# Kernel tuning notes

Measured on AMD Instinct MI355X. Metric: run time of the kernel, lower is better.

The kernel has to match this reference:

```python
import jax, jax.numpy as jnp
import numpy as np
import math

B, LQ, LK = 8, 1024, 1024
D_MODEL, NHEAD = 512, 8
DH = D_MODEL // NHEAD
FACTOR = 5
U = FACTOR * int(np.ceil(np.log(LQ)))  # 35: Informer's sample_k == n_top here (L_Q == L_K)


def _ln(x, g, b, eps=1e-5):
    m = x.mean(-1, keepdims=True)
    v = ((x - m) ** 2).mean(-1, keepdims=True)
    return (x - m) / jnp.sqrt(v + eps) * g + b


def _heads(x):  # (B,L,D) -> (B,H,L,Dh)
    Bx, L, _ = x.shape
    return x.reshape(Bx, L, NHEAD, DH).transpose(0, 2, 1, 3)


def _merge(x):  # (B,H,L,Dh) -> (B,L,D)
    Bx, H, L, Dh = x.shape
    return x.transpose(0, 2, 1, 3).reshape(Bx, L, H * Dh)


def _prob_attn(q, k, v, index_sample):
    # Informer ProbAttention, mask_flag=False. q,k,v: (B,H,L,Dh)
    Bx, H, Lq, Dh = q.shape
    Lk = k.shape[2]
    k_samp = k[:, :, index_sample, :]                        # (B,H,Lq,U,Dh) gathered keys
    qk_samp = jnp.einsum('bhld,bhlud->bhlu', q, k_samp)      # sampled scores
    M = qk_samp.max(-1) - qk_samp.sum(-1) / Lk               # sparsity measurement (B,H,Lq)
    _, top = jax.lax.top_k(M, U)                             # (B,H,U) top-u query indices
    q_red = jnp.take_along_axis(q, top[..., None], axis=2)   # (B,H,U,Dh)
    scores = jnp.einsum('bhud,bhkd->bhuk', q_red, k) * (1.0 / math.sqrt(Dh))
    attn = jax.nn.softmax(scores, axis=-1)
    upd = jnp.einsum('bhuk,bhkd->bhud', attn, v)             # (B,H,U,Dh)
    # initial context = mean of V (non-causal branch), then scatter top-u rows
    ctx = jnp.broadcast_to(v.mean(2, keepdims=True), (Bx, H, Lq, Dh))
    bi = jnp.arange(Bx)[:, None, None]
    hi = jnp.arange(H)[None, :, None]
    ctx = ctx.at[bi, hi, top].set(upd)
    return ctx


def _full_attn(q, k, v):
    s = jnp.einsum('bhld,bhsd->bhls', q, k) * (1.0 / math.sqrt(q.shape[-1]))
    a = jax.nn.softmax(s, axis=-1)
    return jnp.einsum('bhls,bhsd->bhld', a, v)


def setup_inputs():
    key = jax.random.key(0)
    ks = jax.random.split(key, 40)
    d = {}
    d['tgt'] = jax.random.normal(ks[0], (B, LQ, D_MODEL), jnp.float32)
    d['memory'] = jax.random.normal(ks[1], (B, LK, D_MODEL), jnp.float32)
    d['index_sample'] = jax.random.randint(ks[2], (LQ, U), 0, LK)
    i = 3
    for pre in ('1', '2'):
        for n in ('q', 'k', 'v', 'o'):
            d['w%s%s' % (n, pre)] = jax.random.normal(ks[i], (D_MODEL, D_MODEL), jnp.float32) * 0.02
            d['b%s%s' % (n, pre)] = jnp.zeros((D_MODEL,), jnp.float32)
            i += 1
    d['conv1_w'] = jax.random.normal(ks[i], (D_MODEL, 4 * D_MODEL), jnp.float32) * 0.02; i += 1
    d['conv1_b'] = jnp.zeros((4 * D_MODEL,), jnp.float32)
    d['conv2_w'] = jax.random.normal(ks[i], (4 * D_MODEL, D_MODEL), jnp.float32) * 0.02; i += 1
    d['conv2_b'] = jnp.zeros((D_MODEL,), jnp.float32)
    for n in ('ln1', 'ln2', 'ln3'):
        d[n + '_g'] = jnp.ones((D_MODEL,), jnp.float32)
        d[n + '_b'] = jnp.zeros((D_MODEL,), jnp.float32)
    return d


def reference(tgt, memory, index_sample, wq1, bq1, wk1, bk1, wv1, bv1, wo1, bo1,
              wq2, bq2, wk2, bk2, wv2, bv2, wo2, bo2,
              conv1_w, conv1_b, conv2_w, conv2_b,
              ln1_g, ln1_b, ln2_g, ln2_b, ln3_g, ln3_b):
    # dropout layers are identity (eval mode)
    x = tgt
    q = _heads(x @ wq1 + bq1)
    k = _heads(x @ wk1 + bk1)
    v = _heads(x @ wv1 + bv1)
    xn = _merge(_prob_attn(q, k, v, index_sample)) @ wo1 + bo1   # ProbSparse self-attn
    x = _ln(x + xn, ln1_g, ln1_b)                                # norm_enc1, with residual
    q = _heads(x @ wq2 + bq2)
    k = _heads(memory @ wk2 + bk2)
    v = _heads(memory @ wv2 + bv2)
    x = _merge(_full_attn(q, k, v)) @ wo2 + bo2                  # full cross-attn (no residual, per source)
    y = x = _ln(x, ln2_g, ln2_b)                                 # norm_enc2
    y = jax.nn.relu(y @ conv1_w + conv1_b) @ conv2_w + conv2_b   # conv1x1 FFN
    return _ln(x + y, ln3_g, ln3_b)                              # norm_enc3
```

## Files before the change

### kernel.cpp

```cpp
#include <hip/hip_runtime.h>
#include <hip/hip_bf16.h>
#include <cstdint>

constexpr int Bb  = 8;
constexpr int Ls  = 1024;
constexpr int DM  = 512;
constexpr int NH  = 8;
constexpr int DHd = 64;
constexpr int MR  = Bb * Ls;
constexpr int ZH  = Bb * NH;

typedef __attribute__((ext_vector_type(8))) short short8v;
typedef __attribute__((ext_vector_type(4))) short short4v;
typedef __attribute__((ext_vector_type(4))) float floatx4;

__device__ inline short f2bf(float x) {
  __hip_bfloat16 h = __float2bfloat16(x);
  return *reinterpret_cast<short*>(&h);
}

#define GLOAD_LDS16(g, l)                                                        \
  __builtin_amdgcn_global_load_lds(                                              \
      (const __attribute__((address_space(1))) void*)(g),                        \
      (__attribute__((address_space(3))) void*)(l), 16, 0, 0)

template<int MODE, int RELU>
__global__ __launch_bounds__(256) void k_gemm_mfma(
    const __hip_bfloat16* __restrict__ A, const __hip_bfloat16* __restrict__ Wt,
    const float* __restrict__ bias, const float* __restrict__ bias1,
    const float* __restrict__ bias2,
    void* __restrict__ Cout, void* __restrict__ aux1, void* __restrict__ aux2,
    void* __restrict__ aux3,
    int M, int N, int K)
{
  __shared__ __hip_bfloat16 As[128 * 32];
  __shared__ __hip_bfloat16 Bs[128 * 32];
  const int tid = threadIdx.x;
  const int w = tid >> 6, lane = tid & 63;
  const int wr = w >> 1, wc = w & 1;
  const int bm = blockIdx.x * 128, bn = blockIdx.y * 128;
  const int lrow = lane >> 2;
  const int lcol = (lane & 3) * 8;
  const int fr = lane & 15;
  const int fco = (lane >> 4) * 8;
  const short* Ash = (const short*)As;
  const short* Bsh = (const short*)Bs;

  const int ksl = K / gridDim.z;
  const int kb0 = blockIdx.z * ksl;

  floatx4 acc[4][4] = {};
  for (int k0 = kb0; k0 < kb0 + ksl; k0 += 32) {
#pragma unroll
    for (int i = 0; i < 2; ++i) {
      const int chunk = w * 2 + i;
      GLOAD_LDS16(A  + (size_t)(bm + chunk * 16 + lrow) * K + k0 + lcol,
                  As + chunk * 512);
      GLOAD_LDS16(Wt + (size_t)(bn + chunk * 16 + lrow) * K + k0 + lcol,
                  Bs + chunk * 512);
    }
    __syncthreads();
    short8v a[4], b[4];
#pragma unroll
    for (int mi = 0; mi < 4; ++mi)
      a[mi] = *(const short8v*)(Ash + (wr * 64 + mi * 16 + fr) * 32 + fco);
#pragma unroll
    for (int ni = 0; ni < 4; ++ni)
      b[ni] = *(const short8v*)(Bsh + (wc * 64 + ni * 16 + fr) * 32 + fco);
#pragma unroll
    for (int mi = 0; mi < 4; ++mi)
#pragma unroll
      for (int ni = 0; ni < 4; ++ni)
        acc[mi][ni] = __builtin_amdgcn_mfma_f32_16x16x32_bf16(
            a[mi], b[ni], acc[mi][ni], 0, 0, 0);
    __syncthreads();
  }
#pragma unroll
  for (int ni = 0; ni < 4; ++ni) {
    const int cn = bn + wc * 64 + ni * 16 + fr;
    float bv = 0.f;
    if (MODE == 10) {
      const float* bp = (cn < 512) ? bias : (cn < 1024 ? bias1 : bias2);
      bv = bp[cn & 511];
    } else if (MODE == 11) {
      bv = (cn < 512 ? bias : bias1)[cn & 511];
    } else if (MODE != 20) {
      bv = bias[cn];
    }
#pragma unroll
    for (int mi = 0; mi < 4; ++mi) {
#pragma unroll
      for (int j = 0; j < 4; ++j) {
        const int rm = bm + wr * 64 + mi * 16 + (lane >> 4) * 4 + j;
        float v = acc[mi][ni][j] + bv;
        if (RELU) v = fmaxf(v, 0.f);
        if (MODE == 0) {
          ((float*)Cout)[(size_t)rm * N + cn] = v;
        } else if (MODE == 1) {
          ((__hip_bfloat16*)Cout)[(size_t)rm * N + cn] = __float2bfloat16(v);
        } else if (MODE == 4) {
          ((__hip_bfloat16*)Cout)[(size_t)rm * N + cn] = __float2bfloat16(v * 0.125f);
        } else if (MODE == 10) {
          const int sel = cn >> 9, c = cn & 511;
          if (sel == 2) {
            ((float*)aux2)[(size_t)rm * 512 + c] = v;
          } else {
            float* base = sel ? (float*)aux1 : (float*)Cout;
            const int bb = rm >> 10, l = rm & 1023, hh = c >> 6, dd = c & 63;
            base[(((size_t)(bb * 8 + hh)) * 1024 + l) * 64 + dd] = v;
          }
        } else if (MODE == 11) {
          const int c = cn & 511;
          if (cn < 512) {
            const int cs = (c & ~63) | ((c & 63) ^ ((rm & 7) << 3));
            ((__hip_bfloat16*)Cout)[(size_t)rm * 512 + cs] = __float2bfloat16(v);
          } else {
            const int bb = rm >> 10, l = rm & 1023, hh = c >> 6, dd = c & 63;
            ((__hip_bfloat16*)aux1)[(size_t)((bb * 8 + hh) * 64 + dd) * 1024 +
                                    (l ^ ((dd & 7) << 3))] = __float2bfloat16(v);
          }
        } else if (MODE == 20) {
          float* pz = (float*)(blockIdx.z == 0 ? Cout :
                      blockIdx.z == 1 ? aux1 :
                      blockIdx.z == 2 ? aux2 : aux3);
          pz[(size_t)rm * N + cn] = v;
        }
      }
    }
  }
}

__global__ __launch_bounds__(512) void k_flash2(
    const __hip_bfloat16* __restrict__ Qb,
    const __hip_bfloat16* __restrict__ Kb,
    const __hip_bfloat16* __restrict__ Vt,
    __hip_bfloat16* __restrict__ O)
{
  __shared__ __hip_bfloat16 Ks[2][64 * 64];
  __shared__ __hip_bfloat16 Vs[2][64 * 64];
  __shared__ __hip_bfloat16 Ps[8 * 16 * 72];
  const int tid = threadIdx.x, w = tid >> 6, lane = tid & 63;
  const int g = lane >> 4, r = lane & 15;
  const int z = blockIdx.y, b = z >> 3, h = z & 7;
  const int q0 = blockIdx.x * 128 + w * 16;
  __hip_bfloat16* Pw = Ps + w * 16 * 72;

  const int srow = w * 8 + (lane >> 3);
  const int sseg = lane & 7;

  const short8v qf0 = *(const short8v*)(Qb + (size_t)(b * Ls + q0 + r) * DM + h * DHd + g * 8);
  const short8v qf1 = *(const short8v*)(Qb + (size_t)(b * Ls + q0 + r) * DM + h * DHd + 32 + g * 8);

  floatx4 oacc[4] = {};
  float m_run = -1e30f, l_run = 0.f;

  GLOAD_LDS16(Kb + (size_t)(b * Ls + srow) * DM + h * DHd + sseg * 8, &Ks[0][w * 512]);
  GLOAD_LDS16(Vt + ((size_t)z * DHd + srow) * Ls + sseg * 8, &Vs[0][w * 512]);
  asm volatile("s_waitcnt vmcnt(0)" ::: "memory");
  __builtin_amdgcn_s_barrier();

  int cur = 0;
  for (int t = 0; t < 16; ++t) {
    if (t + 1 < 16) {
      GLOAD_LDS16(Kb + (size_t)(b * Ls + (t + 1) * 64 + srow) * DM + h * DHd + sseg * 8,
                  &Ks[cur ^ 1][w * 512]);
      GLOAD_LDS16(Vt + ((size_t)z * DHd + srow) * Ls + (t + 1) * 64 + sseg * 8,
                  &Vs[cur ^ 1][w * 512]);
    }
    const __hip_bfloat16* Kc = Ks[cur];
    const __hip_bfloat16* Vc = Vs[cur];
    float sv[4][4];
    float tmax = -1e30f;
    __builtin_amdgcn_s_setprio(1);
#pragma unroll
    for (int kt = 0; kt < 4; ++kt) {
      const int key = kt * 16 + r, sw = key & 7;
      short8v a0 = *(const short8v*)(Kc + key * 64 + ((g ^ sw) * 8));
      short8v a1 = *(const short8v*)(Kc + key * 64 + (((4 + g) ^ sw) * 8));
      floatx4 c = {};
      c = __builtin_amdgcn_mfma_f32_16x16x32_bf16(a0, qf0, c, 0, 0, 0);
      c = __builtin_amdgcn_mfma_f32_16x16x32_bf16(a1, qf1, c, 0, 0, 0);
#pragma unroll
      for (int j = 0; j < 4; ++j) {
        float x = c[j];
        sv[kt][j] = x;
        tmax = fmaxf(tmax, x);
      }
    }
    __builtin_amdgcn_s_setprio(0);
    tmax = fmaxf(tmax, __shfl_xor(tmax, 16));
    tmax = fmaxf(tmax, __shfl_xor(tmax, 32));
    float m_new;
    if (__all(tmax <= m_run + 8.0f)) {
      m_new = m_run;
    } else {
      m_new = fmaxf(m_run, tmax);
      const float fac = __expf(m_run - m_new);
      float fj[4];
#pragma unroll
      for (int j = 0; j < 4; ++j) fj[j] = __shfl(fac, (lane & 48) | (g * 4 + j));
#pragma unroll
      for (int ct = 0; ct < 4; ++ct)
#pragma unroll
        for (int j = 0; j < 4; ++j) oacc[ct][j] *= fj[j];
      l_run *= fac;
    }
    float psum = 0.f;
#pragma unroll
    for (int kt = 0; kt < 4; ++kt) {
      short4v pk;
#pragma unroll
      for (int j = 0; j < 4; ++j) {
        float p = __expf(sv[kt][j] - m_new);
        psum += p;
        pk[j] = f2bf(p);
      }
      *(short4v*)(Pw + r * 72 + kt * 16 + g * 4) = pk;
    }
    psum += __shfl_xor(psum, 16);
    psum += __shfl_xor(psum, 32);
    l_run += psum;
    m_run = m_new;
    const short8v pa0 = *(const short8v*)(Pw + r * 72 + g * 8);
    const short8v pa1 = *(const short8v*)(Pw + r * 72 + 32 + g * 8);
    __builtin_amdgcn_s_setprio(1);
#pragma unroll
    for (int ct = 0; ct < 4; ++ct) {
      const int d = ct * 16 + r, sw = d & 7;
      short8v v0 = *(const short8v*)(Vc + d * 64 + ((g ^ sw) * 8));
      short8v v1 = *(const short8v*)(Vc + d * 64 + (((4 + g) ^ sw) * 8));
      oacc[ct] = __builtin_amdgcn_mfma_f32_16x16x32_bf16(pa0, v0, oacc[ct], 0, 0, 0);
      oacc[ct] = __builtin_amdgcn_mfma_f32_16x16x32_bf16(pa1, v1, oacc[ct], 0, 0, 0);
    }
    __builtin_amdgcn_s_setprio(0);
    asm volatile("s_waitcnt vmcnt(0)" ::: "memory");
    __builtin_amdgcn_s_barrier();
    cur ^= 1;
  }
  float li[4];
#pragma unroll
  for (int j = 0; j < 4; ++j)
    li[j] = 1.0f / __shfl(l_run, (lane & 48) | (g * 4 + j));
#pragma unroll
  for (int ct = 0; ct < 4; ++ct)
#pragma unroll
    for (int j = 0; j < 4; ++j)
      O[(size_t)(b * Ls + q0 + g * 4 + j) * DM + h * DHd + ct * 16 + r] =
          __float2bfloat16(oacc[ct][j] * li[j]);
}

__global__ __launch_bounds__(256) void k_cvt2(
    const float* __restrict__ in0, const float* __restrict__ in1,
    __hip_bfloat16* __restrict__ o0, __hip_bfloat16* __restrict__ o1)
{
  const size_t half = (size_t)MR * DM / 4;
  size_t i = (size_t)blockIdx.x * 256 + threadIdx.x;
  const float* in = in0; __hip_bfloat16* out = o0;
  if (i >= half) { i -= half; in = in1; out = o1; }
  float4 v = *reinterpret_cast<const float4*>(in + i * 4);
  short4v o;
  o.x = f2bf(v.x); o.y = f2bf(v.y); o.z = f2bf(v.z); o.w = f2bf(v.w);
  *reinterpret_cast<short4v*>(out + i * 4) = o;
}

struct WcvtArgs { const float* s[10]; __hip_bfloat16* d[10]; };
__global__ __launch_bounds__(256) void k_wcvt_all(WcvtArgs a)
{
  __shared__ float t[32][33];
  const int bid = blockIdx.x, tid = threadIdx.x;
  int widx, K, N, kblk, nblk;
  if (bid < 2048) {
    widx = bid >> 8; const int w2 = bid & 255;
    K = 512; N = 512; kblk = w2 & 15; nblk = w2 >> 4;
  } else if (bid < 3072) {
    widx = 8; const int w2 = bid - 2048;
    K = 512; N = 2048; kblk = w2 & 15; nblk = w2 >> 4;
  } else {
    widx = 9; const int w2 = bid - 3072;
    K = 2048; N = 512; kblk = w2 & 63; nblk = w2 >> 6;
  }
  const float* W = a.s[widx];
  __hip_bfloat16* Wt = a.d[widx];
  const int k0 = kblk * 32, n0 = nblk * 32;
  const int r = tid >> 3, c = (tid & 7) * 4;
  float4 v = *reinterpret_cast<const float4*>(W + (size_t)(k0 + r) * N + n0 + c);
  t[r][c + 0] = v.x; t[r][c + 1] = v.y; t[r][c + 2] = v.z; t[r][c + 3] = v.w;
  __syncthreads();
  short4v o;
  o.x = f2bf(t[c + 0][r]); o.y = f2bf(t[c + 1][r]);
  o.z = f2bf(t[c + 2][r]); o.w = f2bf(t[c + 3][r]);
  *reinterpret_cast<short4v*>(Wt + (size_t)(n0 + r) * K + k0 + c) = o;
}

__global__ __launch_bounds__(256) void k_probflash(
    const float* __restrict__ Qz, const float* __restrict__ Kz,
    const float* __restrict__ Vm, const int* __restrict__ top,
    float* __restrict__ Op, float* __restrict__ Ml, float* __restrict__ Ll,
    int U)
{
  __shared__ float Qs[DHd][64 + 4];
  __shared__ float Ks[DHd][64 + 4];
  __shared__ float Vs[64][64];
  const int bid = blockIdx.x;
  const int swz = (bid & 7) * ((16 * ZH) >> 3) + (bid >> 3);
  const int kc = swz & 15, z = swz >> 4, b = z >> 3, h = z & 7;
  const int tid = threadIdx.x;
  const int k0 = kc * 64;
#pragma unroll
  for (int i = 0; i < 4; ++i) {
    const int idx = tid + (i << 8);
    const int r = idx >> 4, c4 = (idx & 15) << 2;
    int u = r; if (u >= U) u = U - 1;
    const int qr = top[z * U + u];
    float4 q4 = *reinterpret_cast<const float4*>(Qz + ((size_t)z * Ls + qr) * 64 + c4);
    Qs[c4 + 0][r] = q4.x; Qs[c4 + 1][r] = q4.y; Qs[c4 + 2][r] = q4.z; Qs[c4 + 3][r] = q4.w;
    float4 k4 = *reinterpret_cast<const float4*>(Kz + ((size_t)z * Ls + k0 + r) * 64 + c4);
    Ks[c4 + 0][r] = k4.x; Ks[c4 + 1][r] = k4.y; Ks[c4 + 2][r] = k4.z; Ks[c4 + 3][r] = k4.w;
    *reinterpret_cast<float4*>(&Vs[r][c4]) =
        *reinterpret_cast<const float4*>(Vm + ((size_t)(b * Ls + k0 + r)) * DM + h * DHd + c4);
  }
  __syncthreads();
  const int mB = (tid >> 4) << 2, nB = (tid & 15) << 2;
  float acc[4][4] = {};
#pragma unroll
  for (int kk = 0; kk < DHd; ++kk) {
    float4 a4 = *reinterpret_cast<const float4*>(&Qs[kk][mB]);
    float4 b4 = *reinterpret_cast<const float4*>(&Ks[kk][nB]);
    const float av[4] = {a4.x, a4.y, a4.z, a4.w};
#pragma unroll
    for (int i = 0; i < 4; ++i) {
      acc[i][0] += av[i] * b4.x; acc[i][1] += av[i] * b4.y;
      acc[i][2] += av[i] * b4.z; acc[i][3] += av[i] * b4.w;
    }
  }
  __syncthreads();
  float (*Ss)[68] = (float (*)[68])Qs;
#pragma unroll
  for (int i = 0; i < 4; ++i) {
    float4 o;
    o.x = acc[i][0] * 0.125f; o.y = acc[i][1] * 0.125f;
    o.z = acc[i][2] * 0.125f; o.w = acc[i][3] * 0.125f;
    *reinterpret_cast<float4*>(&Ss[mB + i][nB]) = o;
  }
  __syncthreads();
  {
    const int row = tid >> 2, q = tid & 3;
    float mx = -1e30f;
#pragma unroll
    for (int j = 0; j < 16; ++j) mx = fmaxf(mx, Ss[row][q * 16 + j]);
    mx = fmaxf(mx, __shfl_xor(mx, 1));
    mx = fmaxf(mx, __shfl_xor(mx, 2));
    float se = 0.f;
#pragma unroll
    for (int j = 0; j < 16; ++j) {
      float p = __expf(Ss[row][q * 16 + j] - mx);
      Ss[row][q * 16 + j] = p;
      se += p;
    }
    se += __shfl_xor(se, 1);
    se += __shfl_xor(se, 2);
    if (q == 0) {
      Ml[((size_t)kc * ZH + z) * 64 + row] = mx;
      Ll[((size_t)kc * ZH + z) * 64 + row] = se;
    }
  }
  __syncthreads();
  const int d = tid & 63, w = tid >> 6;
  float acc2[16] = {};
  for (int k = 0; k < 64; ++k) {
    const float vk = Vs[k][d];
#pragma unroll
    for (int i = 0; i < 16; ++i)
      acc2[i] += Ss[w * 16 + i][k] * vk;
  }
  float* outb = Op + ((size_t)kc * ZH + z) * 4096;
#pragma unroll
  for (int i = 0; i < 16; ++i)
    outb[(w * 16 + i) * 64 + d] = acc2[i];
}

__global__ __launch_bounds__(256) void k_prob_comb(
    const float* __restrict__ Op, const float* __restrict__ Ml,
    const float* __restrict__ Ll, const int* __restrict__ top,
    __hip_bfloat16* __restrict__ ctx, int U)
{
  __shared__ float wsh[16][64];
  __shared__ float Lsh[64];
  const int z = blockIdx.x, b = z >> 3, h = z & 7;
  const int tid = threadIdx.x;
  if (tid < 64) {
    float M = -1e30f;
#pragma unroll
    for (int c = 0; c < 16; ++c)
      M = fmaxf(M, Ml[((size_t)c * ZH + z) * 64 + tid]);
    float L = 0.f;
#pragma unroll
    for (int c = 0; c < 16; ++c) {
      float wv = __expf(Ml[((size_t)c * ZH + z) * 64 + tid] - M);
      wsh[c][tid] = wv;
      L += wv * Ll[((size_t)c * ZH + z) * 64 + tid];
    }
    Lsh[tid] = L;
  }
  __syncthreads();
  for (int e = tid; e < U * 64; e += 256) {
    const int u = e >> 6, d = e & 63;
    float s = 0.f;
#pragma unroll
    for (int c = 0; c < 16; ++c)
      s += wsh[c][u] * Op[((size_t)c * ZH + z) * 4096 + u * 64 + d];
    const int row = top[z * U + u];
    ctx[((size_t)(b * Ls + row)) * DM + h * DHd + d] =
        __float2bfloat16(s / Lsh[u]);
  }
}

template<int UU>
__global__ __launch_bounds__(256) void k_mscore3(
    const float* __restrict__ Qz, const float* __restrict__ Kz,
    const int* __restrict__ smp, float* __restrict__ Ms)
{
  const int bid = blockIdx.x;
  const int swz = (bid & 7) * 128 + (bid >> 3);
  const int gw = swz * 4 + (threadIdx.x >> 6);
  const int lane = threadIdx.x & 63;
  const int li = lane >> 2, dp = (lane & 3) * 16;
  const int l = (gw & 63) * 16 + li;
  const int z = gw >> 6;
  const float* qb = Qz + ((size_t)z * Ls + l) * 64 + dp;
  const float4 q0 = *(const float4*)(qb);
  const float4 q1 = *(const float4*)(qb + 4);
  const float4 q2 = *(const float4*)(qb + 8);
  const float4 q3 = *(const float4*)(qb + 12);
  int kidx[UU];
#pragma unroll
  for (int u = 0; u < UU; ++u) kidx[u] = smp[l * UU + u];
  const float* kzb = Kz + (size_t)z * Ls * 64 + dp;
  float mx = -1e30f, sm = 0.f;
#pragma unroll
  for (int u = 0; u < UU; ++u) {
    const float* kb = kzb + (size_t)kidx[u] * 64;
    const float4 k0 = *(const float4*)(kb);
    const float4 k1 = *(const float4*)(kb + 4);
    const float4 k2 = *(const float4*)(kb + 8);
    const float4 k3 = *(const float4*)(kb + 12);
    float d = q0.x*k0.x + q0.y*k0.y + q0.z*k0.z + q0.w*k0.w
            + q1.x*k1.x + q1.y*k1.y + q1.z*k1.z + q1.w*k1.w
            + q2.x*k2.x + q2.y*k2.y + q2.z*k2.z + q2.w*k2.w
            + q3.x*k3.x + q3.y*k3.y + q3.z*k3.z + q3.w*k3.w;
    d += __shfl_xor(d, 1);
    d += __shfl_xor(d, 2);
    mx = fmaxf(mx, d);
    sm += d;
  }
  if ((lane & 3) == 0) Ms[z * Ls + l] = mx - sm * (1.0f / Ls);
}

__global__ __launch_bounds__(256) void k_mscore3g(
    const float* __restrict__ Qz, const float* __restrict__ Kz,
    const int* __restrict__ smp, float* __restrict__ Ms, int U)
{
  const int bid = blockIdx.x;
  const int swz = (bid & 7) * 128 + (bid >> 3);
  const int gw = swz * 4 + (threadIdx.x >> 6);
  const int lane = threadIdx.x & 63;
  const int li = lane >> 2, dp = (lane & 3) * 16;
  const int l = (gw & 63) * 16 + li;
  const int z = gw >> 6;
  const float* qb = Qz + ((size_t)z * Ls + l) * 64 + dp;
  const float4 q0 = *(const float4*)(qb);
  const float4 q1 = *(const float4*)(qb + 4);
  const float4 q2 = *(const float4*)(qb + 8);
  const float4 q3 = *(const float4*)(qb + 12);
  const float* kzb = Kz + (size_t)z * Ls * 64 + dp;
  float mx = -1e30f, sm = 0.f;
  for (int u = 0; u < U; ++u) {
    const float* kb = kzb + (size_t)smp[l * U + u] * 64;
    const float4 k0 = *(const float4*)(kb);
    const float4 k1 = *(const float4*)(kb + 4);
    const float4 k2 = *(const float4*)(kb + 8);
    const float4 k3 = *(const float4*)(kb + 12);
    float d = q0.x*k0.x + q0.y*k0.y + q0.z*k0.z + q0.w*k0.w
            + q1.x*k1.x + q1.y*k1.y + q1.z*k1.z + q1.w*k1.w
            + q2.x*k2.x + q2.y*k2.y + q2.z*k2.z + q2.w*k2.w
            + q3.x*k3.x + q3.y*k3.y + q3.z*k3.z + q3.w*k3.w;
    d += __shfl_xor(d, 1);
    d += __shfl_xor(d, 2);
    mx = fmaxf(mx, d);
    sm += d;
  }
  if ((lane & 3) == 0) Ms[z * Ls + l] = mx - sm * (1.0f / Ls);
}

__global__ __launch_bounds__(64) void k_topk_w(
    const float* __restrict__ Ms, int* __restrict__ top, int U)
{
  const int z = blockIdx.x, lane = threadIdx.x;
  float v[16];
#pragma unroll
  for (int j = 0; j < 16; ++j) v[j] = Ms[z * Ls + j * 64 + lane];
  for (int it = 0; it < U; ++it) {
    float bv = -1e30f; int bi = 0x7fffffff;
#pragma unroll
    for (int j = 0; j < 16; ++j) {
      const int idx = j * 64 + lane;
      if (v[j] > bv) { bv = v[j]; bi = idx; }
    }
#pragma unroll
    for (int off = 1; off < 64; off <<= 1) {
      const float ov = __shfl_xor(bv, off);
      const int   oi = __shfl_xor(bi, off);
      if (ov > bv || (ov == bv && oi < bi)) { bv = ov; bi = oi; }
    }
    if (lane == 0) top[z * U + it] = bi;
    if ((bi & 63) == lane) v[bi >> 6] = -1e30f;
  }
}

__global__ __launch_bounds__(256) void k_meanv1(
    const float* __restrict__ Vm, float* __restrict__ mvp)
{
  __shared__ float ps[4][64];
  const int gid = blockIdx.x, z = gid >> 3, c = gid & 7, b = z >> 3, h = z & 7;
  const int d = threadIdx.x & 63, g = threadIdx.x >> 6;
  float s = 0.f;
  const int kb = c * 128 + g * 32;
  for (int k = kb; k < kb + 32; ++k)
    s += Vm[((size_t)(b * Ls + k)) * DM + h * DHd + d];
  ps[g][d] = s;
  __syncthreads();
  if (g == 0) mvp[(z * 8 + c) * 64 + d] = ps[0][d] + ps[1][d] + ps[2][d] + ps[3][d];
}

__global__ __launch_bounds__(256) void k_ctxfillb(
    const float* __restrict__ mvp, __hip_bfloat16* __restrict__ ctx)
{
  const int i = blockIdx.x * 256 + threadIdx.x;
  const int c4 = (i & 127) << 2;
  const int row = i >> 7;
  const int b = row >> 10;
  const int h = c4 >> 6;
  const float* base = mvp + ((b * 8 + h) * 8) * 64 + (c4 & 63);
  float4 a = {0.f, 0.f, 0.f, 0.f};
#pragma unroll
  for (int c = 0; c < 8; ++c) {
    float4 m4 = *reinterpret_cast<const float4*>(base + c * 64);
    a.x += m4.x; a.y += m4.y; a.z += m4.z; a.w += m4.w;
  }
  const float inv = 1.0f / Ls;
  short4v o;
  o.x = f2bf(a.x * inv); o.y = f2bf(a.y * inv);
  o.z = f2bf(a.z * inv); o.w = f2bf(a.w * inv);
  *reinterpret_cast<short4v*>(ctx + (size_t)row * DM + c4) = o;
}

template<int NP>
__global__ __launch_bounds__(256) void k_ln2(
    const float* __restrict__ x0, const float* __restrict__ x1,
    const float* __restrict__ x2, const float* __restrict__ x3,
    const float* __restrict__ res, const float* __restrict__ bias,
    const float* __restrict__ g, const float* __restrict__ be,
    float* __restrict__ outf, __hip_bfloat16* __restrict__ outb)
{
  __shared__ float red[4];
  const int row = blockIdx.x, tid = threadIdx.x;
  const size_t base = (size_t)row * DM;
  float2 v = *reinterpret_cast<const float2*>(x0 + base + tid * 2);
  if (NP > 1) {
    float2 a = *reinterpret_cast<const float2*>(x1 + base + tid * 2);
    v.x += a.x; v.y += a.y;
  }
  if (NP > 2) {
    float2 a = *reinterpret_cast<const float2*>(x2 + base + tid * 2);
    v.x += a.x; v.y += a.y;
  }
  if (NP > 3) {
    float2 a = *reinterpret_cast<const float2*>(x3 + base + tid * 2);
    v.x += a.x; v.y += a.y;
  }
  if (bias) {
    float2 a = *reinterpret_cast<const float2*>(bias + tid * 2);
    v.x += a.x; v.y += a.y;
  }
  if (res) {
    float2 r2 = *reinterpret_cast<const float2*>(res + base + tid * 2);
    v.x += r2.x; v.y += r2.y;
  }
  float s = v.x + v.y;
#pragma unroll
  for (int off = 32; off; off >>= 1) s += __shfl_xor(s, off);
  if ((tid & 63) == 0) red[tid >> 6] = s;
  __syncthreads();
  s = red[0] + red[1] + red[2] + red[3];
  const float mean = s * (1.0f / DM);
  __syncthreads();
  float dx = v.x - mean, dy = v.y - mean;
  float q = dx * dx + dy * dy;
#pragma unroll
  for (int off = 32; off; off >>= 1) q += __shfl_xor(q, off);
  if ((tid & 63) == 0) red[tid >> 6] = q;
  __syncthreads();
  q = red[0] + red[1] + red[2] + red[3];
  const float inv = rsqrtf(q * (1.0f / DM) + 1e-5f);
  float2 gg = *reinterpret_cast<const float2*>(g + tid * 2);
  float2 bb = *reinterpret_cast<const float2*>(be + tid * 2);
  float ox = dx * inv * gg.x + bb.x;
  float oy = dy * inv * gg.y + bb.y;
  if (outf) {
    float2 o; o.x = ox; o.y = oy;
    *reinterpret_cast<float2*>(outf + base + tid * 2) = o;
  }
  if (outb) {
    short2 ob; ob.x = f2bf(ox); ob.y = f2bf(oy);
    *reinterpret_cast<short2*>(outb + base + tid * 2) = ob;
  }
}

extern "C" void kernel_launch(void* const* d_in, const int* in_sizes, int n_in,
                              void* d_out, int out_size, void* d_ws, size_t ws_size,
                              hipStream_t stream)
{
  const float* tgt = (const float*)d_in[0];
  const float* mem = (const float*)d_in[1];
  const int*   smp = (const int*)d_in[2];
  const float* wq1 = (const float*)d_in[3];  const float* bq1 = (const float*)d_in[4];
  const float* wk1 = (const float*)d_in[5];  const float* bk1 = (const float*)d_in[6];
  const float* wv1 = (const float*)d_in[7];  const float* bv1 = (const float*)d_in[8];
  const float* wo1 = (const float*)d_in[9];  const float* bo1 = (const float*)d_in[10];
  const float* wq2 = (const float*)d_in[11]; const float* bq2 = (const float*)d_in[12];
  const float* wk2 = (const float*)d_in[13]; const float* bk2 = (const float*)d_in[14];
  const float* wv2 = (const float*)d_in[15]; const float* bv2 = (const float*)d_in[16];
  const float* wo2 = (const float*)d_in[17]; const float* bo2 = (const float*)d_in[18];
  const float* c1w = (const float*)d_in[19]; const float* c1b = (const float*)d_in[20];
  const float* c2w = (const float*)d_in[21]; const float* c2b = (const float*)d_in[22];
  const float* g1  = (const float*)d_in[23]; const float* be1 = (const float*)d_in[24];
  const float* g2  = (const float*)d_in[25]; const float* be2 = (const float*)d_in[26];
  const float* g3  = (const float*)d_in[27]; const float* be3 = (const float*)d_in[28];
  float* outp = (float*)d_out;

  const int U   = in_sizes[2] / Ls;

  char* ws = (char*)d_ws;
  const size_t SZ = (size_t)MR * DM * sizeof(float);
  float* Qz   = (float*)(ws);
  float* Kz   = (float*)(ws + SZ);
  float* W0   = Qz;
  float* W1   = Kz;
  float* W2   = (float*)(ws + 2 * SZ);
  float* Sbuf = (float*)(ws + 3 * SZ);
  float* Op   = Sbuf + (size_t)ZH * 64 * Ls;
  __hip_bfloat16* Tb  = (__hip_bfloat16*)(ws + 5 * SZ);
  __hip_bfloat16* Mb  = (__hip_bfloat16*)(ws + 5 * SZ + SZ / 2);
  __hip_bfloat16* Xb  = (__hip_bfloat16*)(ws + 6 * SZ);
  __hip_bfloat16* Vtb = (__hip_bfloat16*)(ws + 6 * SZ + SZ / 2);
  __hip_bfloat16* Wt3 = Vtb;
  float* CP2 = (float*)(ws + 5 * SZ);
  float* CP3 = (float*)(ws + 6 * SZ);
  char* tail = ws + 7 * SZ;
  __hip_bfloat16* wo1b = (__hip_bfloat16*)tail; tail += DM * DM * 2;
  __hip_bfloat16* wq2b = (__hip_bfloat16*)tail; tail += DM * DM * 2;
  __hip_bfloat16* wk2b = (__hip_bfloat16*)tail; tail += DM * DM * 2;
  __hip_bfloat16* wv2b = (__hip_bfloat16*)tail; tail += DM * DM * 2;
  __hip_bfloat16* wo2b = (__hip_bfloat16*)tail; tail += DM * DM * 2;
  __hip_bfloat16* c1wb = (__hip_bfloat16*)tail; tail += DM * 4 * DM * 2;
  __hip_bfloat16* c2wb = (__hip_bfloat16*)tail; tail += DM * 4 * DM * 2;
  float* Ms  = (float*)tail; tail += (size_t)ZH * Ls * 4;
  int*   top = (int*)tail;   tail += (size_t)ZH * 64 * 4;
  float* mvp = (float*)tail; tail += (size_t)ZH * 8 * DHd * 4;
  float* Ml  = (float*)tail; tail += (size_t)16 * ZH * 64 * 4;
  float* Ll  = (float*)tail; tail += (size_t)16 * ZH * 64 * 4;
  __hip_bfloat16* Kb = Tb;
  __hip_bfloat16* Qb = (__hip_bfloat16*)d_out;
  __hip_bfloat16* hb = (__hip_bfloat16*)Sbuf;

  k_cvt2<<<dim3(2 * MR * DM / 4 / 256), 256, 0, stream>>>(tgt, mem, Tb, Mb);
  WcvtArgs wa;
  wa.s[0] = wq1; wa.d[0] = Wt3;
  wa.s[1] = wk1; wa.d[1] = Wt3 + DM * DM;
  wa.s[2] = wv1; wa.d[2] = Wt3 + 2 * DM * DM;
  wa.s[3] = wo1; wa.d[3] = wo1b;
  wa.s[4] = wq2; wa.d[4] = wq2b;
  wa.s[5] = wk2; wa.d[5] = wk2b;
  wa.s[6] = wv2; wa.d[6] = wv2b;
  wa.s[7] = wo2; wa.d[7] = wo2b;
  wa.s[8] = c1w; wa.d[8] = c1wb;
  wa.s[9] = c2w; wa.d[9] = c2wb;
  k_wcvt_all<<<dim3(4096), 256, 0, stream>>>(wa);

  k_gemm_mfma<10, 0><<<dim3(MR / 128, 12), 256, 0, stream>>>(
      Tb, Wt3, bq1, bk1, bv1, Qz, Kz, W2, nullptr, MR, 1536, DM);

  if (U == 35)
    k_mscore3<35><<<dim3(1024), 256, 0, stream>>>(Qz, Kz, smp, Ms);
  else
    k_mscore3g<<<dim3(1024), 256, 0, stream>>>(Qz, Kz, smp, Ms, U);
  k_topk_w<<<dim3(ZH), 64, 0, stream>>>(Ms, top, U);
  k_probflash<<<dim3(16 * ZH), 256, 0, stream>>>(Qz, Kz, W2, top, Op, Ml, Ll, U);
  k_meanv1<<<dim3(ZH * 8), 256, 0, stream>>>(W2, mvp);
  k_ctxfillb<<<dim3(MR * DM / 4 / 256), 256, 0, stream>>>(mvp, Xb);
  k_prob_comb<<<dim3(ZH), 256, 0, stream>>>(Op, Ml, Ll, top, Xb, U);

  dim3 gsq(MR / 128, DM / 128);
  k_gemm_mfma<20, 0><<<dim3(MR / 128, DM / 128, 2), 256, 0, stream>>>(
      Xb, wo1b, nullptr, nullptr, nullptr, W0, W1, nullptr, nullptr, MR, DM, DM);
  k_ln2<2><<<dim3(MR), 256, 0, stream>>>(W0, W1, nullptr, nullptr,
                                         tgt, bo1, g1, be1, nullptr, Xb);

  k_gemm_mfma<4, 0><<<gsq, 256, 0, stream>>>(
      Xb, wq2b, bq2, nullptr, nullptr, Qb, nullptr, nullptr, nullptr, MR, DM, DM);
  k_gemm_mfma<11, 0><<<dim3(MR / 128, 8), 256, 0, stream>>>(
      Mb, wk2b, bk2, bv2, nullptr, Kb, Vtb, nullptr, nullptr, MR, 1024, DM);

  k_flash2<<<dim3(Ls / 128, ZH), 512, 0, stream>>>(Qb, Kb, Vtb, Xb);

  k_gemm_mfma<20, 0><<<dim3(MR / 128, DM / 128, 2), 256, 0, stream>>>(
      Xb, wo2b, nullptr, nullptr, nullptr, W0, W2, nullptr, nullptr, MR, DM, DM);
  k_ln2<2><<<dim3(MR), 256, 0, stream>>>(W0, W2, nullptr, nullptr,
                                         nullptr, bo2, g2, be2, W1, Xb);

  k_gemm_mfma<1, 1><<<dim3(MR / 128, 4 * DM / 128), 256, 0, stream>>>(
      Xb, c1wb, c1b, nullptr, nullptr, hb, nullptr, nullptr, nullptr, MR, 4 * DM, DM);
  k_gemm_mfma<20, 0><<<dim3(MR / 128, DM / 128, 4), 256, 0, stream>>>(
      hb, c2wb, nullptr, nullptr, nullptr, W0, W2, CP2, CP3, MR, DM, 2 * DM * 2);
  k_ln2<4><<<dim3(MR), 256, 0, stream>>>(W0, W2, CP2, CP3,
                                         W1, c2b, g3, be3, outp, nullptr);
}
```

Before: 369.8 us.

## Fuse conversions and Q/KV projections, use bf16 copies for sparsity scoring

Three changes. The activation and weight fp32-to-bf16 conversion kernels merge into one launch. The QKV projection now also writes bf16 copies of Q and K, so the sparsity-measurement kernel gathers half as many bytes, using 8 lanes per row. The cross-attention Q projection and the memory K/V projection run as one GEMM launch that picks its A source by column block. This trims launches and gather bandwidth, but adds extra bf16 stores in the first GEMM, and bf16 scores could change the top-k query selection.

```diff
diff --git a/kernel.cpp b/kernel.cpp
--- a/kernel.cpp
+++ b/kernel.cpp
@@ -17,6 +17,9 @@
 __device__ inline short f2bf(float x) {
   __hip_bfloat16 h = __float2bfloat16(x);
   return *reinterpret_cast<short*>(&h);
+}
+__device__ inline float bf2f(short s) {
+  return __uint_as_float(((uint32_t)(uint16_t)s) << 16);
 }
 
 #define GLOAD_LDS16(g, l)                                                        \
@@ -46,6 +49,9 @@
   const short* Ash = (const short*)As;
   const short* Bsh = (const short*)Bs;
 
+  const __hip_bfloat16* Asrc = A;
+  if (MODE == 12 && bn >= 512) Asrc = (const __hip_bfloat16*)aux3;
+
   const int ksl = K / gridDim.z;
   const int kb0 = blockIdx.z * ksl;
 
@@ -54,7 +60,7 @@
 #pragma unroll
     for (int i = 0; i < 2; ++i) {
       const int chunk = w * 2 + i;
-      GLOAD_LDS16(A  + (size_t)(bm + chunk * 16 + lrow) * K + k0 + lcol,
+      GLOAD_LDS16(Asrc + (size_t)(bm + chunk * 16 + lrow) * K + k0 + lcol,
                   As + chunk * 512);
       GLOAD_LDS16(Wt + (size_t)(bn + chunk * 16 + lrow) * K + k0 + lcol,
                   Bs + chunk * 512);
@@ -79,11 +85,9 @@
   for (int ni = 0; ni < 4; ++ni) {
     const int cn = bn + wc * 64 + ni * 16 + fr;
     float bv = 0.f;
-    if (MODE == 10) {
+    if (MODE == 10 || MODE == 12) {
       const float* bp = (cn < 512) ? bias : (cn < 1024 ? bias1 : bias2);
       bv = bp[cn & 511];
-    } else if (MODE == 11) {
-      bv = (cn < 512 ? bias : bias1)[cn & 511];
     } else if (MODE != 20) {
       bv = bias[cn];
     }
@@ -94,29 +98,32 @@
         const int rm = bm + wr * 64 + mi * 16 + (lane >> 4) * 4 + j;
         float v = acc[mi][ni][j] + bv;
         if (RELU) v = fmaxf(v, 0.f);
-        if (MODE == 0) {
-          ((float*)Cout)[(size_t)rm * N + cn] = v;
-        } else if (MODE == 1) {
+        if (MODE == 1) {
           ((__hip_bfloat16*)Cout)[(size_t)rm * N + cn] = __float2bfloat16(v);
-        } else if (MODE == 4) {
-          ((__hip_bfloat16*)Cout)[(size_t)rm * N + cn] = __float2bfloat16(v * 0.125f);
         } else if (MODE == 10) {
           const int sel = cn >> 9, c = cn & 511;
           if (sel == 2) {
             ((float*)aux2)[(size_t)rm * 512 + c] = v;
           } else {
+            const int bb = rm >> 10, l = rm & 1023, hh = c >> 6, dd = c & 63;
+            const size_t ci = (((size_t)(bb * 8 + hh)) * 1024 + l) * 64 + dd;
             float* base = sel ? (float*)aux1 : (float*)Cout;
-            const int bb = rm >> 10, l = rm & 1023, hh = c >> 6, dd = c & 63;
-            base[(((size_t)(bb * 8 + hh)) * 1024 + l) * 64 + dd] = v;
+            base[ci] = v;
+            __hip_bfloat16* bb16 = (__hip_bfloat16*)aux3 +
+                                   (sel ? (size_t)ZH * Ls * 64 : 0);
+            bb16[ci] = __float2bfloat16(v);
           }
-        } else if (MODE == 11) {
-          const int c = cn & 511;
-          if (cn < 512) {
+        } else if (MODE == 12) {
+          const int sel = cn >> 9, c = cn & 511;
+          if (sel == 0) {
+            ((__hip_bfloat16*)Cout)[(size_t)rm * 512 + c] =
+                __float2bfloat16(v * 0.125f);
+          } else if (sel == 1) {
             const int cs = (c & ~63) | ((c & 63) ^ ((rm & 7) << 3));
-            ((__hip_bfloat16*)Cout)[(size_t)rm * 512 + cs] = __float2bfloat16(v);
+            ((__hip_bfloat16*)aux1)[(size_t)rm * 512 + cs] = __float2bfloat16(v);
           } else {
             const int bb = rm >> 10, l = rm & 1023, hh = c >> 6, dd = c & 63;
-            ((__hip_bfloat16*)aux1)[(size_t)((bb * 8 + hh) * 64 + dd) * 1024 +
+            ((__hip_bfloat16*)aux2)[(size_t)((bb * 8 + hh) * 64 + dd) * 1024 +
                                     (l ^ ((dd & 7) << 3))] = __float2bfloat16(v);
           }
         } else if (MODE == 20) {
@@ -249,34 +256,32 @@
           __float2bfloat16(oacc[ct][j] * li[j]);
 }
 
-__global__ __launch_bounds__(256) void k_cvt2(
-    const float* __restrict__ in0, const float* __restrict__ in1,
-    __hip_bfloat16* __restrict__ o0, __hip_bfloat16* __restrict__ o1)
-{
-  const size_t half = (size_t)MR * DM / 4;
-  size_t i = (size_t)blockIdx.x * 256 + threadIdx.x;
-  const float* in = in0; __hip_bfloat16* out = o0;
-  if (i >= half) { i -= half; in = in1; out = o1; }
-  float4 v = *reinterpret_cast<const float4*>(in + i * 4);
-  short4v o;
-  o.x = f2bf(v.x); o.y = f2bf(v.y); o.z = f2bf(v.z); o.w = f2bf(v.w);
-  *reinterpret_cast<short4v*>(out + i * 4) = o;
-}
-
-struct WcvtArgs { const float* s[10]; __hip_bfloat16* d[10]; };
-__global__ __launch_bounds__(256) void k_wcvt_all(WcvtArgs a)
-{
+struct CvtArgs { const float* s[12]; __hip_bfloat16* d[12]; };
+__global__ __launch_bounds__(256) void k_cvt_all(CvtArgs a)
+{
+  const int bid = blockIdx.x, tid = threadIdx.x;
+  if (bid < 8192) {
+    const size_t half = (size_t)MR * DM / 4;
+    size_t i = (size_t)bid * 256 + tid;
+    const float* in = a.s[10]; __hip_bfloat16* out = a.d[10];
+    if (i >= half) { i -= half; in = a.s[11]; out = a.d[11]; }
+    float4 v = *reinterpret_cast<const float4*>(in + i * 4);
+    short4v o;
+    o.x = f2bf(v.x); o.y = f2bf(v.y); o.z = f2bf(v.z); o.w = f2bf(v.w);
+    *reinterpret_cast<short4v*>(out + i * 4) = o;
+    return;
+  }
   __shared__ float t[32][33];
-  const int bid = blockIdx.x, tid = threadIdx.x;
+  const int wb = bid - 8192;
   int widx, K, N, kblk, nblk;
-  if (bid < 2048) {
-    widx = bid >> 8; const int w2 = bid & 255;
+  if (wb < 2048) {
+    widx = wb >> 8; const int w2 = wb & 255;
     K = 512; N = 512; kblk = w2 & 15; nblk = w2 >> 4;
-  } else if (bid < 3072) {
-    widx = 8; const int w2 = bid - 2048;
+  } else if (wb < 3072) {
+    widx = 8; const int w2 = wb - 2048;
     K = 512; N = 2048; kblk = w2 & 15; nblk = w2 >> 4;
   } else {
-    widx = 9; const int w2 = bid - 3072;
+    widx = 9; const int w2 = wb - 3072;
     K = 2048; N = 512; kblk = w2 & 63; nblk = w2 >> 6;
   }
   const float* W = a.s[widx];
@@ -416,80 +421,72 @@
 }
 
 template<int UU>
-__global__ __launch_bounds__(256) void k_mscore3(
-    const float* __restrict__ Qz, const float* __restrict__ Kz,
+__global__ __launch_bounds__(256) void k_mscore4(
+    const __hip_bfloat16* __restrict__ Qzb, const __hip_bfloat16* __restrict__ Kzb,
     const int* __restrict__ smp, float* __restrict__ Ms)
 {
   const int bid = blockIdx.x;
-  const int swz = (bid & 7) * 128 + (bid >> 3);
+  const int swz = (bid & 7) * 256 + (bid >> 3);
   const int gw = swz * 4 + (threadIdx.x >> 6);
   const int lane = threadIdx.x & 63;
-  const int li = lane >> 2, dp = (lane & 3) * 16;
-  const int l = (gw & 63) * 16 + li;
-  const int z = gw >> 6;
-  const float* qb = Qz + ((size_t)z * Ls + l) * 64 + dp;
-  const float4 q0 = *(const float4*)(qb);
-  const float4 q1 = *(const float4*)(qb + 4);
-  const float4 q2 = *(const float4*)(qb + 8);
-  const float4 q3 = *(const float4*)(qb + 12);
+  const int li = lane >> 3, dp = (lane & 7) * 8;
+  const int l = (gw & 127) * 8 + li;
+  const int z = gw >> 7;
+  const short8v q8 = *(const short8v*)(Qzb + ((size_t)z * Ls + l) * 64 + dp);
+  float qf[8];
+#pragma unroll
+  for (int j = 0; j < 8; ++j) qf[j] = bf2f(q8[j]);
   int kidx[UU];
 #pragma unroll
   for (int u = 0; u < UU; ++u) kidx[u] = smp[l * UU + u];
-  const float* kzb = Kz + (size_t)z * Ls * 64 + dp;
+  const __hip_bfloat16* kzb = Kzb + (size_t)z * Ls * 64 + dp;
   float mx = -1e30f, sm = 0.f;
 #pragma unroll
   for (int u = 0; u < UU; ++u) {
-    const float* kb = kzb + (size_t)kidx[u] * 64;
-    const float4 k0 = *(const float4*)(kb);
-    const float4 k1 = *(const float4*)(kb + 4);
-    const float4 k2 = *(const float4*)(kb + 8);
-    const float4 k3 = *(const float4*)(kb + 12);
-    float d = q0.x*k0.x + q0.y*k0.y + q0.z*k0.z + q0.w*k0.w
-            + q1.x*k1.x + q1.y*k1.y + q1.z*k1.z + q1.w*k1.w
-            + q2.x*k2.x + q2.y*k2.y + q2.z*k2.z + q2.w*k2.w
-            + q3.x*k3.x + q3.y*k3.y + q3.z*k3.z + q3.w*k3.w;
+    const short8v k8 = *(const short8v*)(kzb + (size_t)kidx[u] * 64);
+    float d = qf[0] * bf2f(k8[0]) + qf[1] * bf2f(k8[1])
+            + qf[2] * bf2f(k8[2]) + qf[3] * bf2f(k8[3])
+            + qf[4] * bf2f(k8[4]) + qf[5] * bf2f(k8[5])
+            + qf[6] * bf2f(k8[6]) + qf[7] * bf2f(k8[7]);
     d += __shfl_xor(d, 1);
     d += __shfl_xor(d, 2);
+    d += __shfl_xor(d, 4);
     mx = fmaxf(mx, d);
     sm += d;
   }
-  if ((lane & 3) == 0) Ms[z * Ls + l] = mx - sm * (1.0f / Ls);
-}
-
-__global__ __launch_bounds__(256) void k_mscore3g(
-    const float* __restrict__ Qz, const float* __restrict__ Kz,
+  if ((lane & 7) == 0) Ms[z * Ls + l] = mx - sm * (1.0f / Ls);
+}
+
+__global__ __launch_bounds__(256) void k_mscore4g(
+    const __hip_bfloat16* __restrict__ Qzb, const __hip_bfloat16* __restrict__ Kzb,
     const int* __restrict__ smp, float* __restrict__ Ms, int U)
 {
   const int bid = blockIdx.x;
-  const int swz = (bid & 7) * 128 + (bid >> 3);
+  const int swz = (bid & 7) * 256 + (bid >> 3);
   const int gw = swz * 4 + (threadIdx.x >> 6);
   const int lane = threadIdx.x & 63;
-  const int li = lane >> 2, dp = (lane & 3) * 16;
-  const int l = (gw & 63) * 16 + li;
-  const int z = gw >> 6;
-  const float* qb = Qz + ((size_t)z * Ls + l) * 64 + dp;
-  const float4 q0 = *(const float4*)(qb);
-  const float4 q1 = *(const float4*)(qb + 4);
-  const float4 q2 = *(const float4*)(qb + 8);
-  const float4 q3 = *(const float4*)(qb + 12);
-  const float* kzb = Kz + (size_t)z * Ls * 64 + dp;
+  const int li = lane >> 3, dp = (lane & 7) * 8;
+  const int l = (gw & 127) * 8 + li;
+  const int z = gw >> 7;
+  const short8v q8 = *(const short8v*)(Qzb + ((size_t)z * Ls + l) * 64 + dp);
+  float qf[8];
+#pragma unroll
+  for (int j = 0; j < 8; ++j) qf[j] = bf2f(q8[j]);
+  const __hip_bfloat16* kzb = Kzb + (size_t)z * Ls * 64 + dp;
   float mx = -1e30f, sm = 0.f;
   for (int u = 0; u < U; ++u) {
-    const float* kb = kzb + (size_t)smp[l * U + u] * 64;
-    const float4 k0 = *(const float4*)(kb);
-    const float4 k1 = *(const float4*)(kb + 4);
-    const float4 k2 = *(const float4*)(kb + 8);
-    const float4 k3 = *(const float4*)(kb + 12);
-    float d = q0.x*k0.x + q0.y*k0.y + q0.z*k0.z + q0.w*k0.w
-            + q1.x*k1.x + q1.y*k1.y + q1.z*k1.z + q1.w*k1.w
-            + q2.x*k2.x + q2.y*k2.y + q2.z*k2.z + q2.w*k2.w
-            + q3.x*k3.x + q3.y*k3.y + q3.z*k3.z + q3.w*k3.w;
+    const short8v k8 = *(const short8v*)(kzb + (size_t)smp[l * U + u] * 64);
+    float d = qf[0] * bf2f(k8[0]) + qf[1] * bf2f(k8[1])
+            + qf[2] * bf2f(k8[2]) + qf[3] * bf2f(k8[3])
+            + qf[4] * bf2f(k8[4]) + qf[5] * bf2f(k8[5])
+            + qf[6] * bf2f(k8[6]) + qf[7] * bf2f(k8[7]);
     d += __shfl_xor(d, 1);
     d += __shfl_xor(d, 2);
+    d += __shfl_xor(d, 4);
     mx = fmaxf(mx, d);
     sm += d;
   }
-  if ((lane & 3) == 0) Ms[z * Ls + l] = mx - sm * (1.0f / Ls);
+  if ((lane & 7) == 0) Ms[z * Ls + l] = mx - sm * (1.0f / Ls);
 }
 
 __global__ __launch_bounds__(64) void k_topk_w(
@@ -649,6 +646,9 @@
   float* W2   = (float*)(ws + 2 * SZ);
   float* Sbuf = (float*)(ws + 3 * SZ);
   float* Op   = Sbuf + (size_t)ZH * 64 * Ls;
+  __hip_bfloat16* QKzb = (__hip_bfloat16*)Sbuf;
+  __hip_bfloat16* Qzb = QKzb;
+  __hip_bfloat16* Kzb = QKzb + (size_t)ZH * Ls * 64;
   __hip_bfloat16* Tb  = (__hip_bfloat16*)(ws + 5 * SZ);
   __hip_bfloat16* Mb  = (__hip_bfloat16*)(ws + 5 * SZ + SZ / 2);
   __hip_bfloat16* Xb  = (__hip_bfloat16*)(ws + 6 * SZ);
@@ -673,43 +673,41 @@
   __hip_bfloat16* Qb = (__hip_bfloat16*)d_out;
   __hip_bfloat16* hb = (__hip_bfloat16*)Sbuf;
 
-  k_cvt2<<<dim3(2 * MR * DM / 4 / 256), 256, 0, stream>>>(tgt, mem, Tb, Mb);
-  WcvtArgs wa;
-  wa.s[0] = wq1; wa.d[0] = Wt3;
-  wa.s[1] = wk1; wa.d[1] = Wt3 + DM * DM;
-  wa.s[2] = wv1; wa.d[2] = Wt3 + 2 * DM * DM;
-  wa.s[3] = wo1; wa.d[3] = wo1b;
-  wa.s[4] = wq2; wa.d[4] = wq2b;
-  wa.s[5] = wk2; wa.d[5] = wk2b;
-  wa.s[6] = wv2; wa.d[6] = wv2b;
-  wa.s[7] = wo2; wa.d[7] = wo2b;
-  wa.s[8] = c1w; wa.d[8] = c1wb;
-  wa.s[9] = c2w; wa.d[9] = c2wb;
-  k_wcvt_all<<<dim3(4096), 256, 0, stream>>>(wa);
+  CvtArgs ca;
+  ca.s[0] = wq1; ca.d[0] = Wt3;
+  ca.s[1] = wk1; ca.d[1] = Wt3 + DM * DM;
+  ca.s[2] = wv1; ca.d[2] = Wt3 + 2 * DM * DM;
+  ca.s[3] = wo1; ca.d[3] = wo1b;
+  ca.s[4] = wq2; ca.d[4] = wq2b;
+  ca.s[5] = wk2; ca.d[5] = wk2b;
+  ca.s[6] = wv2; ca.d[6] = wv2b;
+  ca.s[7] = wo2; ca.d[7] = wo2b;
+  ca.s[8] = c1w; ca.d[8] = c1wb;
+  ca.s[9] = c2w; ca.d[9] = c2wb;
+  ca.s[10] = tgt; ca.d[10] = Tb;
+  ca.s[11] = mem; ca.d[11] = Mb;
+  k_cvt_all<<<dim3(12288), 256, 0, stream>>>(ca);
 
   k_gemm_mfma<10, 0><<<dim3(MR / 128, 12), 256, 0, stream>>>(
-      Tb, Wt3, bq1, bk1, bv1, Qz, Kz, W2, nullptr, MR, 1536, DM);
+      Tb, Wt3, bq1, bk1, bv1, Qz, Kz, W2, QKzb, MR, 1536, DM);
 
   if (U == 35)
-    k_mscore3<35><<<dim3(1024), 256, 0, stream>>>(Qz, Kz, smp, Ms);
+    k_mscore4<35><<<dim3(2048), 256, 0, stream>>>(Qzb, Kzb, smp, Ms);
   else
-    k_mscore3g<<<dim3(1024), 256, 0, stream>>>(Qz, Kz, smp, Ms, U);
+    k_mscore4g<<<dim3(2048), 256, 0, stream>>>(Qzb, Kzb, smp, Ms, U);
   k_topk_w<<<dim3(ZH), 64, 0, stream>>>(Ms, top, U);
   k_probflash<<<dim3(16 * ZH), 256, 0, stream>>>(Qz, Kz, W2, top, Op, Ml, Ll, U);
   k_meanv1<<<dim3(ZH * 8), 256, 0, stream>>>(W2, mvp);
   k_ctxfillb<<<dim3(MR * DM / 4 / 256), 256, 0, stream>>>(mvp, Xb);
   k_prob_comb<<<dim3(ZH), 256, 0, stream>>>(Op, Ml, Ll, top, Xb, U);
 
-  dim3 gsq(MR / 128, DM / 128);
   k_gemm_mfma<20, 0><<<dim3(MR / 128, DM / 128, 2), 256, 0, stream>>>(
       Xb, wo1b, nullptr, nullptr, nullptr, W0, W1, nullptr, nullptr, MR, DM, DM);
   k_ln2<2><<<dim3(MR), 256, 0, stream>>>(W0, W1, nullptr, nullptr,
                                          tgt, bo1, g1, be1, nullptr, Xb);
 
-  k_gemm_mfma<4, 0><<<gsq, 256, 0, stream>>>(
-      Xb, wq2b, bq2, nullptr, nullptr, Qb, nullptr, nullptr, nullptr, MR, DM, DM);
-  k_gemm_mfma<11, 0><<<dim3(MR / 128, 8), 256, 0, stream>>>(
-      Mb, wk2b, bk2, bv2, nullptr, Kb, Vtb, nullptr, nullptr, MR, 1024, DM);
+  k_gemm_mfma<12, 0><<<dim3(MR / 128, 12), 256, 0, stream>>>(
+      Xb, wq2b, bq2, bk2, bv2, Qb, Kb, Vtb, (void*)Mb, MR, 1536, DM);
 
   k_flash2<<<dim3(Ls / 128, ZH), 512, 0, stream>>>(Qb, Kb, Vtb, Xb);
 
```

After: 345.5 us. 1.07x faster.
